# Kernel optimization log

Measured on AMD Instinct MI355X. Metric: run time of the kernel, lower is better.

Reference implementation:

```python
import jax, jax.numpy as jnp
import numpy as np

N, T, D = 64, 1024, 64  # (batch*heads, seq_len==max_len, head_dim)
PADDING_NUM = -2.0**32 + 1.0


def setup_inputs() -> dict:
    key = jax.random.key(0)
    kq, kk, kv = jax.random.split(key, 3)
    q = jax.random.normal(kq, (N, T, D), dtype=jnp.float32)
    k = jax.random.normal(kk, (N, T, D), dtype=jnp.float32)
    v = jax.random.normal(kv, (N, T, D), dtype=jnp.float32)
    return {"q": q, "k": k, "v": v}


def reference(q, k, v):
    # attn = q @ k^T / sqrt(d_k)  -> (N, T_q, T_k)
    dk_norm = jnp.sqrt(jnp.asarray(k.shape[-1], dtype=jnp.float32))
    scores = jnp.einsum('bqd,bkd->bqk', q, k) / dk_norm
    # key padding mask: keys whose abs-sum is 0 are masked to padding_num
    key_mask = (jnp.sum(jnp.abs(k), axis=-1) != 0)[:, None, :]  # (N, 1, T_k)
    scores = jnp.where(key_mask, scores, PADDING_NUM)
    # causal (future) mask: cumsum of eye -> lower triangular keep-mask
    causal = jnp.tril(jnp.ones((T, T), dtype=bool))[None, :, :]  # (1, T, T)
    scores = jnp.where(causal, scores, PADDING_NUM)
    attn = jax.nn.softmax(scores, axis=-1)
    # dropout with training=False is identity
    return jnp.einsum('bqk,bkv->bqv', attn, v)
```

## Files before the change

kernel.cpp:

```cpp
#include <hip/hip_runtime.h>
#include <hip/hip_bf16.h>
#include <math.h>


#define N_HEADS 64
#define T_SEQ   1024
#define D_HEAD  64
#define KVB     64
#define PADDING_NUM (-4294967295.0f)
#define KSTRIDE 144
#define VSTRIDE 144
#define QSCALE  (0.125f * 1.4426950408889634f)

typedef __attribute__((ext_vector_type(8)))  short bf16x8;
typedef __attribute__((ext_vector_type(16))) float f32x16;
typedef __attribute__((ext_vector_type(4)))  unsigned int uint4v;

union FragU { uint4v u; bf16x8 v; };

template<bool B> struct BoolC { static constexpr bool value = B; };

static __device__ __forceinline__ unsigned pk2(float lo, float hi) {
    union { __hip_bfloat162 h2; unsigned u; } c;
    c.h2 = __float22bfloat162_rn(make_float2(lo, hi));
    return c.u;
}
static __device__ __forceinline__ f32x16 zero16() {
    f32x16 z;
    #pragma unroll
    for (int i = 0; i < 16; ++i) z[i] = 0.f;
    return z;
}

__global__ __launch_bounds__(256)
void attn_fwd(const float* __restrict__ q, const float* __restrict__ k,
              const float* __restrict__ v, float* __restrict__ out) {
    __shared__ __align__(16) char  KT_lds[2][KVB * KSTRIDE];
    __shared__ __align__(16) char  VT_lds[2][D_HEAD * VSTRIDE];
    __shared__ __align__(16) float kadd[2][KVB];

    const int bx  = blockIdx.x;
    const int n   = bx & 63;
    const int pr  = bx >> 6;
    const int tid = threadIdx.x;
    const int w   = tid >> 6;
    const int l   = tid & 63;
    const int h   = l >> 5;
    const int ql  = l & 31;
    const int sel  = (w ^ bx) & 1;
    const int hs   = sel ? pr : (15 - pr);
    const int qrow = hs * 64 + (w >> 1) * 32 + ql;

    const float* qg = q + (size_t)n * T_SEQ * D_HEAD;
    const float* kg = k + (size_t)n * T_SEQ * D_HEAD;
    const float* vg = v + (size_t)n * T_SEQ * D_HEAD;

    FragU qf[4];
    #pragma unroll
    for (int s = 0; s < 4; ++s) {
        const float* qp = qg + (size_t)qrow * D_HEAD + s * 16 + h * 8;
        float4 a = ((const float4*)qp)[0], b = ((const float4*)qp)[1];
        qf[s].u[0] = pk2(a.x * QSCALE, a.y * QSCALE);
        qf[s].u[1] = pk2(a.z * QSCALE, a.w * QSCALE);
        qf[s].u[2] = pk2(b.x * QSCALE, b.y * QSCALE);
        qf[s].u[3] = pk2(b.z * QSCALE, b.w * QSCALE);
    }

    f32x16 O0 = zero16(), O1 = zero16();
    float m = -INFINITY, l_sum = 0.f;

    float4 kbuf[2][2], vbuf[2][2];
    auto k_issue = [&](int t) {
        const float* base = kg + (size_t)t * KVB * D_HEAD;
        #pragma unroll
        for (int i = 0; i < 2; ++i) {
            int c = tid + 256 * i; int key = c >> 3, oct = c & 7;
            const float4* p = (const float4*)(base + key * D_HEAD + oct * 8);
            kbuf[i][0] = p[0]; kbuf[i][1] = p[1];
        }
    };
    auto v_issue = [&](int t) {
        const float* base = vg + (size_t)t * KVB * D_HEAD;
        #pragma unroll
        for (int i = 0; i < 2; ++i) {
            int c = tid + 256 * i; int kp = c & 31, dq = c >> 5;
            const float* p0 = base + (2 * kp) * D_HEAD + dq * 4;
            vbuf[i][0] = *(const float4*)p0;
            vbuf[i][1] = *(const float4*)(p0 + D_HEAD);
        }
    };
    auto kv_write = [&](int b) {
        #pragma unroll
        for (int i = 0; i < 2; ++i) {
            int c = tid + 256 * i; int key = c >> 3, oct = c & 7;
            float4 A = kbuf[i][0], B = kbuf[i][1];
            float s = fabsf(A.x) + fabsf(A.y) + fabsf(A.z) + fabsf(A.w)
                    + fabsf(B.x) + fabsf(B.y) + fabsf(B.z) + fabsf(B.w);
            s += __shfl_xor(s, 1); s += __shfl_xor(s, 2); s += __shfl_xor(s, 4);
            if (oct == 0) kadd[b][key] = (s != 0.f) ? 0.f : PADDING_NUM;
            uint4v w4;
            w4[0] = pk2(A.x, A.y); w4[1] = pk2(A.z, A.w);
            w4[2] = pk2(B.x, B.y); w4[3] = pk2(B.z, B.w);
            *(uint4v*)(KT_lds[b] + key * KSTRIDE + oct * 16) = w4;

            int kp = c & 31, dq = c >> 5;
            float4 VA = vbuf[i][0], VB = vbuf[i][1];
            *(unsigned*)(VT_lds[b] + (dq * 4 + 0) * VSTRIDE + kp * 4) = pk2(VA.x, VB.x);
            *(unsigned*)(VT_lds[b] + (dq * 4 + 1) * VSTRIDE + kp * 4) = pk2(VA.y, VB.y);
            *(unsigned*)(VT_lds[b] + (dq * 4 + 2) * VSTRIDE + kp * 4) = pk2(VA.z, VB.z);
            *(unsigned*)(VT_lds[b] + (dq * 4 + 3) * VSTRIDE + kp * 4) = pk2(VA.w, VB.w);
        }
    };

    auto process = [&](int b, int t, auto causal_c) {
        constexpr bool CAUSAL = decltype(causal_c)::value;
        const char* Kb = KT_lds[b];
        const char* Vb = VT_lds[b];

        f32x16 S[2];
        #pragma unroll
        for (int kgi = 0; kgi < 2; ++kgi) {
            f32x16 acc = zero16();
            #pragma unroll
            for (int s = 0; s < 4; ++s) {
                bf16x8 kf = *(const bf16x8*)(Kb + (kgi * 32 + ql) * KSTRIDE + s * 32 + h * 16);
                acc = __builtin_amdgcn_mfma_f32_32x32x16_bf16(kf, qf[s].v, acc, 0, 0, 0);
            }
            S[kgi] = acc;
        }

        float tmax = -INFINITY;
        #pragma unroll
        for (int kgi = 0; kgi < 2; ++kgi) {
            #pragma unroll
            for (int rq = 0; rq < 4; ++rq) {
                float4 kd = *(const float4*)&kadd[b][kgi * 32 + rq * 8 + 4 * h];
                #pragma unroll
                for (int j = 0; j < 4; ++j) {
                    int r = rq * 4 + j;
                    float sc = S[kgi][r] + ((const float*)&kd)[j];
                    if (CAUSAL) {
                        int key = t * KVB + kgi * 32 + rq * 8 + 4 * h + j;
                        sc = (key <= qrow) ? sc : PADDING_NUM;
                    }
                    S[kgi][r] = sc;
                    tmax = fmaxf(tmax, sc);
                }
            }
        }
        tmax = fmaxf(tmax, __shfl_xor(tmax, 32));

        const float newm = fmaxf(m, tmax);
        const float corr = __builtin_amdgcn_exp2f(m - newm);
        m = newm;
        l_sum *= corr;
        #pragma unroll
        for (int i = 0; i < 16; ++i) { O0[i] *= corr; O1[i] *= corr; }

        float ls = 0.f;
        #pragma unroll
        for (int kgi = 0; kgi < 2; ++kgi)
            #pragma unroll
            for (int r = 0; r < 16; ++r) {
                float p = __builtin_amdgcn_exp2f(S[kgi][r] - newm);
                S[kgi][r] = p;
                ls += p;
            }
        ls += __shfl_xor(ls, 32);
        l_sum += ls;

        #pragma unroll
        for (int kgi = 0; kgi < 2; ++kgi) {
            #pragma unroll
            for (int s2 = 0; s2 < 2; ++s2) {
                unsigned A0 = pk2(S[kgi][8 * s2 + 0], S[kgi][8 * s2 + 1]);
                unsigned A1 = pk2(S[kgi][8 * s2 + 2], S[kgi][8 * s2 + 3]);
                unsigned A2 = pk2(S[kgi][8 * s2 + 4], S[kgi][8 * s2 + 5]);
                unsigned A3 = pk2(S[kgi][8 * s2 + 6], S[kgi][8 * s2 + 7]);
                unsigned sw0 = (unsigned)__shfl_xor((int)A0, 32);
                unsigned sw1 = (unsigned)__shfl_xor((int)A1, 32);
                unsigned sw2 = (unsigned)__shfl_xor((int)A2, 32);
                unsigned sw3 = (unsigned)__shfl_xor((int)A3, 32);
                FragU pb;
                pb.u[0] = h ? sw2 : A0;
                pb.u[1] = h ? sw3 : A1;
                pb.u[2] = h ? A2 : sw0;
                pb.u[3] = h ? A3 : sw1;
                const int ksf = kgi * 2 + s2;
                bf16x8 vf0 = *(const bf16x8*)(Vb + (0 * 32 + ql) * VSTRIDE + ksf * 32 + h * 16);
                bf16x8 vf1 = *(const bf16x8*)(Vb + (1 * 32 + ql) * VSTRIDE + ksf * 32 + h * 16);
                O0 = __builtin_amdgcn_mfma_f32_32x32x16_bf16(vf0, pb.v, O0, 0, 0, 0);
                O1 = __builtin_amdgcn_mfma_f32_32x32x16_bf16(vf1, pb.v, O1, 0, 0, 0);
            }
        }
    };

    k_issue(0); v_issue(0);
    kv_write(0);
    __syncthreads();

    const int nt = 16 - pr;
    int buf = 0;
    for (int t = 0; t < nt; ++t) {
        if (t + 1 < nt) { k_issue(t + 1); v_issue(t + 1); }
        if (t < hs)       process(buf, t, BoolC<false>{});
        else if (t == hs) process(buf, t, BoolC<true>{});
        if (t + 1 < nt) kv_write(buf ^ 1);
        __syncthreads();
        buf ^= 1;
    }

    const float inv = 1.f / l_sum;
    #pragma unroll
    for (int g = 0; g < 2; ++g) {
        #pragma unroll
        for (int r = 0; r < 16; ++r) {
            int d = (r & 3) + 8 * (r >> 2) + 4 * h + 32 * g;
            float val = (g ? O1[r] : O0[r]) * inv;
            out[(size_t)n * T_SEQ * D_HEAD + (size_t)qrow * D_HEAD + d] = val;
        }
    }
}

extern "C" void kernel_launch(void* const* d_in, const int* in_sizes, int n_in,
                              void* d_out, int out_size, void* d_ws, size_t ws_size,
                              hipStream_t stream) {
    (void)d_ws; (void)ws_size; (void)in_sizes; (void)n_in; (void)out_size;
    const float* q = (const float*)d_in[0];
    const float* k = (const float*)d_in[1];
    const float* v = (const float*)d_in[2];
    float* o = (float*)d_out;
    dim3 grid(N_HEADS * 8);
    dim3 block(256);
    hipLaunchKernelGGL(attn_fwd, grid, block, 0, stream, q, k, v, o);
}
```

Baseline: 46.71 us.

## Give each wave private K/V LDS tiles, drop block barriers, add lazy rescaling

Each wave now owns its own 32-row query strip, drawn from a balanced causal assignment of strips. It loads and converts its own K/V tiles into a private LDS region, so every __syncthreads in the main loop goes away. Softmax rescaling of the accumulators is skipped unless the running max grows by more than a threshold. Output stores are vectorized to float4, and launch bounds now ask for 2 blocks per CU. In exchange, each block fetches K/V four times over from L2, and the large per-thread prefetch buffers raise register pressure.

```diff
diff --git a/kernel.cpp b/kernel.cpp
--- a/kernel.cpp
+++ b/kernel.cpp
@@ -11,12 +11,19 @@
 #define KSTRIDE 144
 #define VSTRIDE 144
 #define QSCALE  (0.125f * 1.4426950408889634f)
+#define RESCALE_THR 8.0f
+#define KBYTES  (KVB * KSTRIDE)
+#define VBYTES  (D_HEAD * VSTRIDE)
+#define WAVE_LDS (KBYTES + VBYTES + 256)
+
+#define LGKM0 asm volatile("s_waitcnt lgkmcnt(0)" ::: "memory")
 
 typedef __attribute__((ext_vector_type(8)))  short bf16x8;
 typedef __attribute__((ext_vector_type(16))) float f32x16;
 typedef __attribute__((ext_vector_type(4)))  unsigned int uint4v;
 
 union FragU { uint4v u; bf16x8 v; };
+union F4U  { float4 f; uint4v u; };
 
 template<bool B> struct BoolC { static constexpr bool value = B; };
 
@@ -32,24 +39,29 @@
     return z;
 }
 
-__global__ __launch_bounds__(256)
+__global__ __launch_bounds__(256, 2)
 void attn_fwd(const float* __restrict__ q, const float* __restrict__ k,
               const float* __restrict__ v, float* __restrict__ out) {
-    __shared__ __align__(16) char  KT_lds[2][KVB * KSTRIDE];
-    __shared__ __align__(16) char  VT_lds[2][D_HEAD * VSTRIDE];
-    __shared__ __align__(16) float kadd[2][KVB];
+    __shared__ __align__(16) char lds[4][WAVE_LDS];
 
     const int bx  = blockIdx.x;
     const int n   = bx & 63;
-    const int pr  = bx >> 6;
+    const int g   = bx >> 6;
     const int tid = threadIdx.x;
     const int w   = tid >> 6;
     const int l   = tid & 63;
     const int h   = l >> 5;
     const int ql  = l & 31;
-    const int sel  = (w ^ bx) & 1;
-    const int hs   = sel ? pr : (15 - pr);
-    const int qrow = hs * 64 + (w >> 1) * 32 + ql;
+
+    const int widx = (w + (n & 3)) & 3;
+    const int sp   = (widx == 0) ? g : (widx == 1) ? (31 - g)
+                   : (widx == 2) ? (15 - g) : (16 + g);
+    const int qrow = sp * 32 + ql;
+    const int nt   = (sp >> 1) + 1;
+
+    char*  Kl    = lds[w];
+    char*  Vt    = lds[w] + KBYTES;
+    float* kaddL = (float*)(lds[w] + KBYTES + VBYTES);
 
     const float* qg = q + (size_t)n * T_SEQ * D_HEAD;
     const float* kg = k + (size_t)n * T_SEQ * D_HEAD;
@@ -67,74 +79,72 @@
     }
 
     f32x16 O0 = zero16(), O1 = zero16();
-    float m = -INFINITY, l_sum = 0.f;
-
-    float4 kbuf[2][2], vbuf[2][2];
+    float mx = -INFINITY, lsum = 0.f;
+
+    float4 kb[16], vb[16];
     auto k_issue = [&](int t) {
-        const float* base = kg + (size_t)t * KVB * D_HEAD;
-        #pragma unroll
-        for (int i = 0; i < 2; ++i) {
-            int c = tid + 256 * i; int key = c >> 3, oct = c & 7;
-            const float4* p = (const float4*)(base + key * D_HEAD + oct * 8);
-            kbuf[i][0] = p[0]; kbuf[i][1] = p[1];
+        const float4* p = (const float4*)(kg + (size_t)t * KVB * D_HEAD + l * D_HEAD);
+        #pragma unroll
+        for (int i = 0; i < 16; ++i) kb[i] = p[i];
+    };
+    auto k_write = [&]() {
+        LGKM0;
+        unsigned ob = 0u;
+        #pragma unroll
+        for (int i = 0; i < 16; ++i) {
+            F4U c; c.f = kb[i];
+            ob |= c.u[0] | c.u[1] | c.u[2] | c.u[3];
+        }
+        kaddL[l] = ((ob & 0x7fffffffu) != 0u) ? 0.f : PADDING_NUM;
+        #pragma unroll
+        for (int o = 0; o < 8; ++o) {
+            uint4v w4;
+            w4[0] = pk2(kb[2*o].x,   kb[2*o].y);
+            w4[1] = pk2(kb[2*o].z,   kb[2*o].w);
+            w4[2] = pk2(kb[2*o+1].x, kb[2*o+1].y);
+            w4[3] = pk2(kb[2*o+1].z, kb[2*o+1].w);
+            *(uint4v*)(Kl + l * KSTRIDE + o * 16) = w4;
         }
     };
     auto v_issue = [&](int t) {
-        const float* base = vg + (size_t)t * KVB * D_HEAD;
-        #pragma unroll
-        for (int i = 0; i < 2; ++i) {
-            int c = tid + 256 * i; int kp = c & 31, dq = c >> 5;
-            const float* p0 = base + (2 * kp) * D_HEAD + dq * 4;
-            vbuf[i][0] = *(const float4*)p0;
-            vbuf[i][1] = *(const float4*)(p0 + D_HEAD);
-        }
-    };
-    auto kv_write = [&](int b) {
-        #pragma unroll
-        for (int i = 0; i < 2; ++i) {
-            int c = tid + 256 * i; int key = c >> 3, oct = c & 7;
-            float4 A = kbuf[i][0], B = kbuf[i][1];
-            float s = fabsf(A.x) + fabsf(A.y) + fabsf(A.z) + fabsf(A.w)
-                    + fabsf(B.x) + fabsf(B.y) + fabsf(B.z) + fabsf(B.w);
-            s += __shfl_xor(s, 1); s += __shfl_xor(s, 2); s += __shfl_xor(s, 4);
-            if (oct == 0) kadd[b][key] = (s != 0.f) ? 0.f : PADDING_NUM;
-            uint4v w4;
-            w4[0] = pk2(A.x, A.y); w4[1] = pk2(A.z, A.w);
-            w4[2] = pk2(B.x, B.y); w4[3] = pk2(B.z, B.w);
-            *(uint4v*)(KT_lds[b] + key * KSTRIDE + oct * 16) = w4;
-
-            int kp = c & 31, dq = c >> 5;
-            float4 VA = vbuf[i][0], VB = vbuf[i][1];
-            *(unsigned*)(VT_lds[b] + (dq * 4 + 0) * VSTRIDE + kp * 4) = pk2(VA.x, VB.x);
-            *(unsigned*)(VT_lds[b] + (dq * 4 + 1) * VSTRIDE + kp * 4) = pk2(VA.y, VB.y);
-            *(unsigned*)(VT_lds[b] + (dq * 4 + 2) * VSTRIDE + kp * 4) = pk2(VA.z, VB.z);
-            *(unsigned*)(VT_lds[b] + (dq * 4 + 3) * VSTRIDE + kp * 4) = pk2(VA.w, VB.w);
-        }
-    };
-
-    auto process = [&](int b, int t, auto causal_c) {
+        const float* base = vg + (size_t)t * KVB * D_HEAD + (size_t)(2 * ql) * D_HEAD + 32 * h;
+        #pragma unroll
+        for (int i = 0; i < 8; ++i) {
+            vb[i]     = ((const float4*)base)[i];
+            vb[i + 8] = ((const float4*)(base + D_HEAD))[i];
+        }
+    };
+    auto v_write = [&]() {
+        LGKM0;
+        #pragma unroll
+        for (int i = 0; i < 8; ++i) {
+            const int d0 = 32 * h + 4 * i;
+            float4 A = vb[i], B = vb[i + 8];
+            *(unsigned*)(Vt + (d0 + 0) * VSTRIDE + ql * 4) = pk2(A.x, B.x);
+            *(unsigned*)(Vt + (d0 + 1) * VSTRIDE + ql * 4) = pk2(A.y, B.y);
+            *(unsigned*)(Vt + (d0 + 2) * VSTRIDE + ql * 4) = pk2(A.z, B.z);
+            *(unsigned*)(Vt + (d0 + 3) * VSTRIDE + ql * 4) = pk2(A.w, B.w);
+        }
+    };
+
+    auto qk_soft = [&](f32x16 (&S)[2], int t, auto causal_c) {
         constexpr bool CAUSAL = decltype(causal_c)::value;
-        const char* Kb = KT_lds[b];
-        const char* Vb = VT_lds[b];
-
-        f32x16 S[2];
         #pragma unroll
         for (int kgi = 0; kgi < 2; ++kgi) {
             f32x16 acc = zero16();
             #pragma unroll
             for (int s = 0; s < 4; ++s) {
-                bf16x8 kf = *(const bf16x8*)(Kb + (kgi * 32 + ql) * KSTRIDE + s * 32 + h * 16);
+                bf16x8 kf = *(const bf16x8*)(Kl + (kgi * 32 + ql) * KSTRIDE + s * 32 + h * 16);
                 acc = __builtin_amdgcn_mfma_f32_32x32x16_bf16(kf, qf[s].v, acc, 0, 0, 0);
             }
             S[kgi] = acc;
         }
-
-        float tmax = -INFINITY;
+        float tm[4] = {-INFINITY, -INFINITY, -INFINITY, -INFINITY};
         #pragma unroll
         for (int kgi = 0; kgi < 2; ++kgi) {
             #pragma unroll
             for (int rq = 0; rq < 4; ++rq) {
-                float4 kd = *(const float4*)&kadd[b][kgi * 32 + rq * 8 + 4 * h];
+                float4 kd = *(const float4*)&kaddL[kgi * 32 + rq * 8 + 4 * h];
                 #pragma unroll
                 for (int j = 0; j < 4; ++j) {
                     int r = rq * 4 + j;
@@ -144,31 +154,34 @@
                         sc = (key <= qrow) ? sc : PADDING_NUM;
                     }
                     S[kgi][r] = sc;
-                    tmax = fmaxf(tmax, sc);
+                    tm[rq] = fmaxf(tm[rq], sc);
                 }
             }
         }
+        float tmax = fmaxf(fmaxf(tm[0], tm[1]), fmaxf(tm[2], tm[3]));
         tmax = fmaxf(tmax, __shfl_xor(tmax, 32));
 
-        const float newm = fmaxf(m, tmax);
-        const float corr = __builtin_amdgcn_exp2f(m - newm);
-        m = newm;
-        l_sum *= corr;
-        #pragma unroll
-        for (int i = 0; i < 16; ++i) { O0[i] *= corr; O1[i] *= corr; }
-
+        if (!__all(tmax <= mx + RESCALE_THR)) {
+            const float newm = fmaxf(mx, tmax);
+            const float corr = __builtin_amdgcn_exp2f(mx - newm);
+            mx = newm;
+            lsum *= corr;
+            #pragma unroll
+            for (int i = 0; i < 16; ++i) { O0[i] *= corr; O1[i] *= corr; }
+        }
         float ls = 0.f;
         #pragma unroll
         for (int kgi = 0; kgi < 2; ++kgi)
             #pragma unroll
             for (int r = 0; r < 16; ++r) {
-                float p = __builtin_amdgcn_exp2f(S[kgi][r] - newm);
-                S[kgi][r] = p;
-                ls += p;
-            }
-        ls += __shfl_xor(ls, 32);
-        l_sum += ls;
-
+                float pv = __builtin_amdgcn_exp2f(S[kgi][r] - mx);
+                S[kgi][r] = pv;
+                ls += pv;
+            }
+        lsum += ls;
+    };
+
+    auto pv_acc = [&](f32x16 (&S)[2]) {
         #pragma unroll
         for (int kgi = 0; kgi < 2; ++kgi) {
             #pragma unroll
@@ -187,8 +200,8 @@
                 pb.u[2] = h ? A2 : sw0;
                 pb.u[3] = h ? A3 : sw1;
                 const int ksf = kgi * 2 + s2;
-                bf16x8 vf0 = *(const bf16x8*)(Vb + (0 * 32 + ql) * VSTRIDE + ksf * 32 + h * 16);
-                bf16x8 vf1 = *(const bf16x8*)(Vb + (1 * 32 + ql) * VSTRIDE + ksf * 32 + h * 16);
+                bf16x8 vf0 = *(const bf16x8*)(Vt + (0 * 32 + ql) * VSTRIDE + ksf * 32 + h * 16);
+                bf16x8 vf1 = *(const bf16x8*)(Vt + (1 * 32 + ql) * VSTRIDE + ksf * 32 + h * 16);
                 O0 = __builtin_amdgcn_mfma_f32_32x32x16_bf16(vf0, pb.v, O0, 0, 0, 0);
                 O1 = __builtin_amdgcn_mfma_f32_32x32x16_bf16(vf1, pb.v, O1, 0, 0, 0);
             }
@@ -196,28 +209,33 @@
     };
 
     k_issue(0); v_issue(0);
-    kv_write(0);
-    __syncthreads();
-
-    const int nt = 16 - pr;
-    int buf = 0;
+    k_write();  v_write();
+
     for (int t = 0; t < nt; ++t) {
-        if (t + 1 < nt) { k_issue(t + 1); v_issue(t + 1); }
-        if (t < hs)       process(buf, t, BoolC<false>{});
-        else if (t == hs) process(buf, t, BoolC<true>{});
-        if (t + 1 < nt) kv_write(buf ^ 1);
-        __syncthreads();
-        buf ^= 1;
+        const bool more = (t + 1 < nt);
+        if (more) k_issue(t + 1);
+        f32x16 S[2];
+        if (t == nt - 1) qk_soft(S, t, BoolC<true>{});
+        else             qk_soft(S, t, BoolC<false>{});
+        if (more) { k_write(); v_issue(t + 1); }
+        pv_acc(S);
+        if (more) v_write();
     }
 
-    const float inv = 1.f / l_sum;
+    const float ltot = lsum + __shfl_xor(lsum, 32);
+    const float inv  = 1.f / ltot;
+    float* op = out + ((size_t)n * T_SEQ + qrow) * D_HEAD;
     #pragma unroll
-    for (int g = 0; g < 2; ++g) {
-        #pragma unroll
-        for (int r = 0; r < 16; ++r) {
-            int d = (r & 3) + 8 * (r >> 2) + 4 * h + 32 * g;
-            float val = (g ? O1[r] : O0[r]) * inv;
-            out[(size_t)n * T_SEQ * D_HEAD + (size_t)qrow * D_HEAD + d] = val;
+    for (int gg = 0; gg < 2; ++gg) {
+        #pragma unroll
+        for (int q2 = 0; q2 < 4; ++q2) {
+            const int d0 = 8 * q2 + 4 * h + 32 * gg;
+            float4 t4;
+            t4.x = (gg ? O1[4*q2+0] : O0[4*q2+0]) * inv;
+            t4.y = (gg ? O1[4*q2+1] : O0[4*q2+1]) * inv;
+            t4.z = (gg ? O1[4*q2+2] : O0[4*q2+2]) * inv;
+            t4.w = (gg ? O1[4*q2+3] : O0[4*q2+3]) * inv;
+            *(float4*)(op + d0) = t4;
         }
     }
 }
```

Result: slower. 79.79 us (+70.8%).
